# Kernel tuning notes

Hardware: AMD Instinct MI355X
Metric: run time of the kernel (lower is better)

## Reference

```python
import jax, jax.numpy as jnp
import numpy as np

HEAD_SIZE = 64
EMBED_DIM = 1024
SEQ_LEN = 4096
BATCH = 4


def setup_inputs() -> dict:
    key = jax.random.key(0)
    kx, kk, kq, kv = jax.random.split(key, 4)
    x = jax.random.normal(kx, (BATCH, SEQ_LEN, EMBED_DIM), dtype=jnp.float32)
    # nn.Linear(embedding_dim, head_size, bias=False): weight [head_size, embed];
    # store transposed [embed, head_size] so projection is x @ W.
    scale = 1.0 / np.sqrt(EMBED_DIM)
    Wk = jax.random.uniform(kk, (EMBED_DIM, HEAD_SIZE), jnp.float32, -scale, scale)
    Wq = jax.random.uniform(kq, (EMBED_DIM, HEAD_SIZE), jnp.float32, -scale, scale)
    Wv = jax.random.uniform(kv, (EMBED_DIM, HEAD_SIZE), jnp.float32, -scale, scale)
    return {"x": x, "Wk": Wk, "Wq": Wq, "Wv": Wv}


def reference(x, Wk, Wq, Wv):
    B, T, C = x.shape
    k = x @ Wk  # [B, T, H]
    q = x @ Wq  # [B, T, H]
    v = x @ Wv  # [B, T, H]
    H = k.shape[-1]
    s = jnp.einsum('bth,bsh->bts', q, k) * (H ** -0.5)  # [B, T, T]
    causal = jnp.tril(jnp.ones((T, T), dtype=bool))
    s = jnp.where(causal, s, -jnp.inf)
    a = jax.nn.softmax(s, axis=-1)  # dropout p=0.0 -> identity
    z = jnp.einsum('bts,bsh->bth', a, v)  # [B, T, H]
    return z
```

## Files before the change

### kernel.cpp

```cpp
#include <hip/hip_runtime.h>

#define SEQ 4096
#define EMB 1024
#define HS 64

typedef __attribute__((ext_vector_type(8))) short bf16x8;
typedef __attribute__((ext_vector_type(4))) float f32x4;

__device__ __forceinline__ unsigned short f2b(float f) {
    union { float f; unsigned u; } v; v.f = f;
    unsigned r = v.u + 0x7fffu + ((v.u >> 16) & 1u);
    return (unsigned short)(r >> 16);
}
__device__ __forceinline__ float b2f(unsigned short h) {
    union { unsigned u; float f; } v; v.u = ((unsigned)h) << 16;
    return v.f;
}
template <typename T>
__device__ __forceinline__ void gll16(const T* g, void* l) {
    __builtin_amdgcn_global_load_lds(
        (const __attribute__((address_space(1))) unsigned int*)(g),
        (__attribute__((address_space(3))) unsigned int*)(l), 16, 0, 0);
}

__global__ __launch_bounds__(256) void wt_kernel(const float* __restrict__ Wq,
                                                 const float* __restrict__ Wk,
                                                 const float* __restrict__ Wv,
                                                 unsigned short* __restrict__ Wt) {
    int id = blockIdx.x * 256 + threadIdx.x;
    int mat = id >> 16;
    int rem = id & 65535;
    int k = rem >> 6;
    int n = rem & 63;
    const float* W = (mat == 0) ? Wq : (mat == 1) ? Wk : Wv;
    float scale = (mat == 0) ? 0.125f * 1.44269504f : 1.0f;
    Wt[(mat * HS + n) * EMB + k] = f2b(W[k * HS + n] * scale);
}

__global__ __launch_bounds__(256, 4) void proj_kernel(const float* __restrict__ x,
                                                      const unsigned short* __restrict__ Wt,
                                                      unsigned short* __restrict__ Qb,
                                                      unsigned short* __restrict__ Kb,
                                                      unsigned short* __restrict__ Vt) {
    __shared__ float xf[2][32 * 64];
    __shared__ unsigned short wb[2][96 * 64];
    const int tid = threadIdx.x;
    const int wave = tid >> 6, lane = tid & 63;
    const int col = lane & 15, quad = lane >> 4;
    const int bid = blockIdx.x;
    const int cls = bid & 1;
    const int m0 = (bid >> 1) * 32;
    const int b = m0 >> 12, t0 = m0 & 4095;
    const int mh = wave & 1;
    const int ngrp = wave >> 1;

    const int xr_in = lane >> 4;
    const int xc = lane & 15;
    const int wr_in = lane >> 3;
    const int wc = lane & 7;

    f32x4 acc[3];
    #pragma unroll
    for (int j = 0; j < 3; j++) acc[j] = (f32x4){0.f, 0.f, 0.f, 0.f};

    auto stage = [&](int k0, int bufi) {
        #pragma unroll
        for (int t = 0; t < 2; t++) {
            int R = (wave + t * 4) * 4;
            int row = R + xr_in;
            gll16(x + (size_t)(m0 + row) * EMB + k0 + ((xc ^ (row & 15)) << 2),
                  &xf[bufi][R * 64]);
        }
        #pragma unroll
        for (int t = 0; t < 3; t++) {
            int R = (wave * 3 + t) * 8;
            int row = R + wr_in;
            gll16(Wt + (size_t)(cls * 96 + row) * EMB + k0 + ((wc ^ (row & 7)) << 3),
                  &wb[bufi][R * 64]);
        }
    };

    stage(0, 0);
    int buf = 0;
    #pragma unroll 1
    for (int k0 = 0; k0 < EMB; k0 += 64) {
        __syncthreads();
        if (k0 + 64 < EMB) stage(k0 + 64, buf ^ 1);
        #pragma unroll
        for (int kc = 0; kc < 2; kc++) {
            const int q2 = quad + kc * 4;
            const int rr = mh * 16 + col;
            float4 lo = *(const float4*)&xf[buf][rr * 64 + (((2 * q2) ^ col) << 2)];
            float4 hi = *(const float4*)&xf[buf][rr * 64 + (((2 * q2 + 1) ^ col) << 2)];
            bf16x8 af;
            af[0] = (short)f2b(lo.x); af[1] = (short)f2b(lo.y);
            af[2] = (short)f2b(lo.z); af[3] = (short)f2b(lo.w);
            af[4] = (short)f2b(hi.x); af[5] = (short)f2b(hi.y);
            af[6] = (short)f2b(hi.z); af[7] = (short)f2b(hi.w);
            #pragma unroll
            for (int nt = 0; nt < 3; nt++) {
                int rn = ngrp * 48 + nt * 16 + col;
                bf16x8 bfr = *(const bf16x8*)&wb[buf][rn * 64 + ((q2 ^ (col & 7)) << 3)];
                acc[nt] = __builtin_amdgcn_mfma_f32_16x16x32_bf16(af, bfr, acc[nt], 0, 0, 0);
            }
        }
        buf ^= 1;
    }

    #pragma unroll
    for (int nt = 0; nt < 3; nt++) {
        const int G = cls * 96 + ngrp * 48 + nt * 16 + col;
        const int mat = G >> 6;
        const int nc = G & 63;
        #pragma unroll
        for (int r = 0; r < 4; r++) {
            unsigned short val = f2b(acc[nt][r]);
            int row = mh * 16 + quad * 4 + r;
            if (mat == 0)      Qb[(size_t)(m0 + row) * HS + nc] = val;
            else if (mat == 1) Kb[(size_t)(m0 + row) * HS + nc] = val;
            else               Vt[((size_t)b * HS + nc) * SEQ + t0 + row] = val;
        }
    }
}

__global__ __launch_bounds__(512, 4) void attn_kernel(const unsigned short* __restrict__ Qb,
                                                      const unsigned short* __restrict__ Kb,
                                                      const unsigned short* __restrict__ Vt,
                                                      unsigned short* __restrict__ Opart,
                                                      float* __restrict__ Lpart) {
    __shared__ unsigned short Kl[2][64 * 64];
    __shared__ unsigned short Vl[2][64 * 64];
    __shared__ unsigned short P_lds[8][16 * 72];
    const int tid = threadIdx.x;
    const int wave = tid >> 6, lane = tid & 63;
    const int col = lane & 15, quad = lane >> 4;
    const int bid = blockIdx.x;
    const int g = 101 - (bid >> 2);
    const int b = bid & 3;
    int T = 0, accp = 0;
    for (;;) { int np = (T + 6) / 6; if (accp + np > g) break; accp += np; T++; }
    const int piece = g - accp;
    const int q0 = T << 7;
    const int s_beg = piece * 12;
    const int s_end = min(s_beg + 12, 2 * T + 2);

    const unsigned short* Kp = Kb + ((size_t)(b << 12)) * HS;
    const unsigned short* Vp = Vt + (size_t)b * HS * SEQ;

    bf16x8 qf[2];
    #pragma unroll
    for (int c = 0; c < 2; c++)
        qf[c] = *(const bf16x8*)(Qb + ((size_t)(b << 12) + q0 + wave * 16 + col) * HS + quad * 8 + c * 32);

    f32x4 o[4];
    float l[4];
    #pragma unroll
    for (int ct = 0; ct < 4; ct++) o[ct] = (f32x4){0.f, 0.f, 0.f, 0.f};
    #pragma unroll
    for (int r = 0; r < 4; r++) l[r] = 0.f;

    const int r_in = lane >> 3;
    const int ch = lane & 7;

    auto stage = [&](int s, int bufi) {
        const int kv0 = s << 6;
        int R = wave * 8;
        int row = R + r_in;
        gll16(Kp + (size_t)(kv0 + row) * HS + ((ch ^ (row & 7)) << 3), &Kl[bufi][R * 64]);
        gll16(Vp + (size_t)row * SEQ + kv0 + ((ch ^ (row & 7)) << 3), &Vl[bufi][R * 64]);
    };

    stage(s_beg, 0);
    int buf = 0;
    const int rgb = q0 + wave * 16 + quad * 4;
    unsigned short* Pl = P_lds[wave];

    #pragma unroll 1
    for (int s = s_beg; s < s_end; s++) {
        __syncthreads();
        if (s + 1 < s_end) stage(s + 1, buf ^ 1);
        const int kv0 = s << 6;

        f32x4 sacc[4];
        #pragma unroll
        for (int ct = 0; ct < 4; ct++) sacc[ct] = (f32x4){0.f, 0.f, 0.f, 0.f};
        #pragma unroll
        for (int ct = 0; ct < 4; ct++) {
            int n = ct * 16 + col;
            #pragma unroll
            for (int kc = 0; kc < 2; kc++) {
                bf16x8 kf = *(const bf16x8*)&Kl[buf][n * 64 + (((kc * 4 + quad) ^ (col & 7)) << 3)];
                sacc[ct] = __builtin_amdgcn_mfma_f32_16x16x32_bf16(qf[kc], kf, sacc[ct], 0, 0, 0);
            }
        }

        float p[4][4];
        #pragma unroll
        for (int ct = 0; ct < 4; ct++) {
            int cg = kv0 + ct * 16 + col;
            #pragma unroll
            for (int r = 0; r < 4; r++) {
                float e = __builtin_exp2f(sacc[ct][r]);
                e = (cg > rgb + r) ? 0.f : e;
                p[ct][r] = e;
                l[r] += e;
            }
        }

        #pragma unroll
        for (int ct = 0; ct < 4; ct++)
            #pragma unroll
            for (int r = 0; r < 4; r++)
                Pl[(quad * 4 + r) * 72 + ct * 16 + col] = f2b(p[ct][r]);
        bf16x8 pf[2];
        #pragma unroll
        for (int c = 0; c < 2; c++)
            pf[c] = *(const bf16x8*)&Pl[col * 72 + quad * 8 + c * 32];

        #pragma unroll
        for (int ct = 0; ct < 4; ct++) {
            int h = ct * 16 + col;
            #pragma unroll
            for (int kc = 0; kc < 2; kc++) {
                bf16x8 vf = *(const bf16x8*)&Vl[buf][h * 64 + (((kc * 4 + quad) ^ (col & 7)) << 3)];
                o[ct] = __builtin_amdgcn_mfma_f32_16x16x32_bf16(pf[kc], vf, o[ct], 0, 0, 0);
            }
        }
        buf ^= 1;
    }

    #pragma unroll
    for (int off = 1; off < 16; off <<= 1)
        #pragma unroll
        for (int r = 0; r < 4; r++)
            l[r] += __shfl_xor(l[r], off, 64);

    const int widx = bid * 8 + wave;
    unsigned short* Op = Opart + (size_t)widx * 1024;
    #pragma unroll
    for (int ct = 0; ct < 4; ct++) {
        ushort4 st;
        st.x = f2b(o[ct][0]); st.y = f2b(o[ct][1]);
        st.z = f2b(o[ct][2]); st.w = f2b(o[ct][3]);
        *(ushort4*)(Op + ct * 256 + lane * 4) = st;
    }
    if (col == 0) {
        #pragma unroll
        for (int r = 0; r < 4; r++)
            Lpart[widx * 16 + quad * 4 + r] = l[r];
    }
}

__global__ __launch_bounds__(256) void comb_kernel(const unsigned short* __restrict__ Opart,
                                                   const float* __restrict__ Lpart,
                                                   float* __restrict__ out) {
    const int bid = blockIdx.x;
    const int b = bid & 3;
    const int T = (bid >> 2) & 31;
    const int wave = bid >> 7;
    const int tid = threadIdx.x;
    const int lane = tid & 63, ct = tid >> 6;
    const int col = lane & 15, quad = lane >> 4;

    const int q = T / 6, r6 = T % 6;
    const int base = (q + 1) * (3 * q + r6);
    const int np = (T + 6) / 6;

    float acc[4] = {0.f, 0.f, 0.f, 0.f};
    float l[4] = {0.f, 0.f, 0.f, 0.f};
    for (int p = 0; p < np; p++) {
        int gg = base + p;
        int bidp = ((101 - gg) << 2) | b;
        int widx = bidp * 8 + wave;
        ushort4 v = *(const ushort4*)(Opart + (size_t)widx * 1024 + ct * 256 + lane * 4);
        acc[0] += b2f(v.x); acc[1] += b2f(v.y);
        acc[2] += b2f(v.z); acc[3] += b2f(v.w);
        #pragma unroll
        for (int r = 0; r < 4; r++)
            l[r] += Lpart[widx * 16 + quad * 4 + r];
    }
    const size_t rowb = (size_t)(b << 12) + (T << 7) + wave * 16 + quad * 4;
    #pragma unroll
    for (int r = 0; r < 4; r++)
        out[(rowb + r) * HS + ct * 16 + col] = acc[r] / l[r];
}

extern "C" void kernel_launch(void* const* d_in, const int* in_sizes, int n_in,
                              void* d_out, int out_size, void* d_ws, size_t ws_size,
                              hipStream_t stream) {
    const float* x  = (const float*)d_in[0];
    const float* Wk = (const float*)d_in[1];
    const float* Wq = (const float*)d_in[2];
    const float* Wv = (const float*)d_in[3];
    float* out = (float*)d_out;

    char* ws = (char*)d_ws;
    unsigned short* Wt = (unsigned short*)(ws);
    unsigned short* Qb = (unsigned short*)(ws + 393216);
    unsigned short* Kb = (unsigned short*)(ws + 2490368);
    unsigned short* Vt = (unsigned short*)(ws + 4587520);
    unsigned short* Opart = (unsigned short*)(ws + 6684672);
    float* Lpart          = (float*)(ws + 13369344);

    wt_kernel<<<dim3(768), dim3(256), 0, stream>>>(Wq, Wk, Wv, Wt);
    proj_kernel<<<dim3(1024), dim3(256), 0, stream>>>(x, Wt, Qb, Kb, Vt);
    attn_kernel<<<dim3(408), dim3(512), 0, stream>>>(Qb, Kb, Vt, Opart, Lpart);
    comb_kernel<<<dim3(1024), dim3(256), 0, stream>>>(Opart, Lpart, out);
}
```

Before: 155.8 us.

## Replace split-KV combine kernel with atomic accumulation and last-arriver finalize

The separate combine kernel is removed. Each attention wave now atomically adds its fp32 partial output and row sums into global accumulators. A per-(batch, tile, wave) counter lets the last arriving piece divide and write the final output. The zeroing of the accumulators and counters is folded into the weight-transpose kernel. This saves one launch and the bf16 partial round trip, at the cost of many float atomics (16 per lane) and fence overhead.

```diff
diff --git a/kernel.cpp b/kernel.cpp
--- a/kernel.cpp
+++ b/kernel.cpp
@@ -11,10 +11,6 @@
     union { float f; unsigned u; } v; v.f = f;
     unsigned r = v.u + 0x7fffu + ((v.u >> 16) & 1u);
     return (unsigned short)(r >> 16);
-}
-__device__ __forceinline__ float b2f(unsigned short h) {
-    union { unsigned u; float f; } v; v.u = ((unsigned)h) << 16;
-    return v.f;
 }
 template <typename T>
 __device__ __forceinline__ void gll16(const T* g, void* l) {
@@ -26,7 +22,8 @@
 __global__ __launch_bounds__(256) void wt_kernel(const float* __restrict__ Wq,
                                                  const float* __restrict__ Wk,
                                                  const float* __restrict__ Wv,
-                                                 unsigned short* __restrict__ Wt) {
+                                                 unsigned short* __restrict__ Wt,
+                                                 float4* __restrict__ zbase) {
     int id = blockIdx.x * 256 + threadIdx.x;
     int mat = id >> 16;
     int rem = id & 65535;
@@ -35,6 +32,8 @@
     const float* W = (mat == 0) ? Wq : (mat == 1) ? Wk : Wv;
     float scale = (mat == 0) ? 0.125f * 1.44269504f : 1.0f;
     Wt[(mat * HS + n) * EMB + k] = f2b(W[k * HS + n] * scale);
+    for (int i = id; i < 266496; i += 196608)
+        zbase[i] = make_float4(0.f, 0.f, 0.f, 0.f);
 }
 
 __global__ __launch_bounds__(256, 4) void proj_kernel(const float* __restrict__ x,
@@ -126,8 +125,10 @@
 __global__ __launch_bounds__(512, 4) void attn_kernel(const unsigned short* __restrict__ Qb,
                                                       const unsigned short* __restrict__ Kb,
                                                       const unsigned short* __restrict__ Vt,
-                                                      unsigned short* __restrict__ Opart,
-                                                      float* __restrict__ Lpart) {
+                                                      float* __restrict__ Oacc,
+                                                      float* __restrict__ Lacc,
+                                                      unsigned int* __restrict__ cnt,
+                                                      float* __restrict__ out) {
     __shared__ unsigned short Kl[2][64 * 64];
     __shared__ unsigned short Vl[2][64 * 64];
     __shared__ unsigned short P_lds[8][16 * 72];
@@ -140,6 +141,7 @@
     int T = 0, accp = 0;
     for (;;) { int np = (T + 6) / 6; if (accp + np > g) break; accp += np; T++; }
     const int piece = g - accp;
+    const int np = (T + 6) / 6;
     const int q0 = T << 7;
     const int s_beg = piece * 12;
     const int s_end = min(s_beg + 12, 2 * T + 2);
@@ -172,6 +174,7 @@
 
     stage(s_beg, 0);
     int buf = 0;
+    const int grb = (b << 12) + q0 + wave * 16;
     const int rgb = q0 + wave * 16 + quad * 4;
     unsigned short* Pl = P_lds[wave];
 
@@ -235,54 +238,32 @@
         for (int r = 0; r < 4; r++)
             l[r] += __shfl_xor(l[r], off, 64);
 
-    const int widx = bid * 8 + wave;
-    unsigned short* Op = Opart + (size_t)widx * 1024;
-    #pragma unroll
-    for (int ct = 0; ct < 4; ct++) {
-        ushort4 st;
-        st.x = f2b(o[ct][0]); st.y = f2b(o[ct][1]);
-        st.z = f2b(o[ct][2]); st.w = f2b(o[ct][3]);
-        *(ushort4*)(Op + ct * 256 + lane * 4) = st;
-    }
+    #pragma unroll
+    for (int ct = 0; ct < 4; ct++)
+        #pragma unroll
+        for (int r = 0; r < 4; r++)
+            atomicAdd(&Oacc[(size_t)(grb + quad * 4 + r) * HS + ct * 16 + col], o[ct][r]);
     if (col == 0) {
         #pragma unroll
         for (int r = 0; r < 4; r++)
-            Lpart[widx * 16 + quad * 4 + r] = l[r];
-    }
-}
-
-__global__ __launch_bounds__(256) void comb_kernel(const unsigned short* __restrict__ Opart,
-                                                   const float* __restrict__ Lpart,
-                                                   float* __restrict__ out) {
-    const int bid = blockIdx.x;
-    const int b = bid & 3;
-    const int T = (bid >> 2) & 31;
-    const int wave = bid >> 7;
-    const int tid = threadIdx.x;
-    const int lane = tid & 63, ct = tid >> 6;
-    const int col = lane & 15, quad = lane >> 4;
-
-    const int q = T / 6, r6 = T % 6;
-    const int base = (q + 1) * (3 * q + r6);
-    const int np = (T + 6) / 6;
-
-    float acc[4] = {0.f, 0.f, 0.f, 0.f};
-    float l[4] = {0.f, 0.f, 0.f, 0.f};
-    for (int p = 0; p < np; p++) {
-        int gg = base + p;
-        int bidp = ((101 - gg) << 2) | b;
-        int widx = bidp * 8 + wave;
-        ushort4 v = *(const ushort4*)(Opart + (size_t)widx * 1024 + ct * 256 + lane * 4);
-        acc[0] += b2f(v.x); acc[1] += b2f(v.y);
-        acc[2] += b2f(v.z); acc[3] += b2f(v.w);
-        #pragma unroll
-        for (int r = 0; r < 4; r++)
-            l[r] += Lpart[widx * 16 + quad * 4 + r];
-    }
-    const size_t rowb = (size_t)(b << 12) + (T << 7) + wave * 16 + quad * 4;
-    #pragma unroll
-    for (int r = 0; r < 4; r++)
-        out[(rowb + r) * HS + ct * 16 + col] = acc[r] / l[r];
+            atomicAdd(&Lacc[grb + quad * 4 + r], l[r]);
+    }
+    __threadfence();
+    const int ci = ((b << 5) + T) * 8 + wave;
+    unsigned int old = 0;
+    if (lane == 0) old = atomicAdd(&cnt[ci], 1u);
+    old = (unsigned int)__shfl((int)old, 0, 64);
+    if (old == (unsigned int)(np - 1)) {
+        __threadfence();
+        #pragma unroll 4
+        for (int i = 0; i < 16; i++) {
+            float v = __hip_atomic_load(&Oacc[(size_t)(grb + i) * HS + lane],
+                                        __ATOMIC_ACQUIRE, __HIP_MEMORY_SCOPE_AGENT);
+            float lv = __hip_atomic_load(&Lacc[grb + i],
+                                         __ATOMIC_ACQUIRE, __HIP_MEMORY_SCOPE_AGENT);
+            out[(size_t)(grb + i) * HS + lane] = v / lv;
+        }
+    }
 }
 
 extern "C" void kernel_launch(void* const* d_in, const int* in_sizes, int n_in,
@@ -299,11 +280,12 @@
     unsigned short* Qb = (unsigned short*)(ws + 393216);
     unsigned short* Kb = (unsigned short*)(ws + 2490368);
     unsigned short* Vt = (unsigned short*)(ws + 4587520);
-    unsigned short* Opart = (unsigned short*)(ws + 6684672);
-    float* Lpart          = (float*)(ws + 13369344);
-
-    wt_kernel<<<dim3(768), dim3(256), 0, stream>>>(Wq, Wk, Wv, Wt);
+    float* Oacc        = (float*)(ws + 6684672);
+    float* Lacc        = (float*)(ws + 10878976);
+    unsigned int* cnt  = (unsigned int*)(ws + 10944512);
+    float4* zbase      = (float4*)(ws + 6684672);
+
+    wt_kernel<<<dim3(768), dim3(256), 0, stream>>>(Wq, Wk, Wv, Wt, zbase);
     proj_kernel<<<dim3(1024), dim3(256), 0, stream>>>(x, Wt, Qb, Kb, Vt);
-    attn_kernel<<<dim3(408), dim3(512), 0, stream>>>(Qb, Kb, Vt, Opart, Lpart);
-    comb_kernel<<<dim3(1024), dim3(256), 0, stream>>>(Opart, Lpart, out);
-}
+    attn_kernel<<<dim3(408), dim3(512), 0, stream>>>(Qb, Kb, Vt, Oacc, Lacc, cnt, out);
+}
```

New measurement: 494.1 us. 3.17x slower.
